# Kernel optimization log

Measured on AMD Instinct MI355X. Metric: run time of the kernel, lower is better.

## Reference

```python
import jax, jax.numpy as jnp
import numpy as np

N, E, M = 20000, 320000, 64
LOG2 = float(np.log(2.0))
INV_SQRT_M = 1.0 / float(np.sqrt(M))
PW_S = float(np.sqrt(1.0 / 5.0))   # path weight for 0e-output paths: sqrt(ir_out.dim / n_paths)
PW_V = float(np.sqrt(3.0 / 5.0))   # path weight for 1e-output paths
INV_SQRT3 = 1.0 / float(np.sqrt(3.0))
INV_SQRT2 = 1.0 / float(np.sqrt(2.0))


def ssp(x):  # ShiftedSoftPlus
    return jax.nn.softplus(x) - LOG2


def split(feat):
    return feat[:, :M], feat[:, M:].reshape(feat.shape[0], M, 3)


def e3_linear(feat, W0, b0, W1):
    # e3nn o3.Linear per irrep group, fan-in normalized; bias only on scalar (0e) irreps
    s, v = split(feat)
    s = s @ (W0 * INV_SQRT_M) + b0
    v = jnp.einsum('nui,uv->nvi', v, W1 * INV_SQRT_M)
    return jnp.concatenate([s, v.reshape(v.shape[0], 3 * M)], axis=-1)


def fcnet(h, Ws):
    # e3nn FullyConnectedNet: no biases, fan-in normalized, ssp between layers
    for i, W in enumerate(Ws):
        h = h @ (W * (1.0 / float(np.sqrt(W.shape[0]))))
        if i < len(Ws) - 1:
            h = ssp(h)
    return h


def setup_inputs() -> dict:
    key = jax.random.key(0)
    ks = jax.random.split(key, 24)
    r = lambda i, shape: jax.random.normal(ks[i], shape, dtype=jnp.float32)
    inp = {
        'x': r(0, (N, 4 * M)),
        'edge_index': jax.random.randint(ks[1], (2, E), 0, N, dtype=jnp.int64)
        if jax.config.jax_enable_x64 else jax.random.randint(ks[1], (2, E), 0, N),
        'edge_sh': r(2, (E, 4)),
        'edge_attr': r(3, (E, 64)),
        # linear_node_pre
        'W_pre0': r(4, (M, M)), 'b_pre0': jnp.zeros((M,), jnp.float32), 'W_pre1': r(5, (M, M)),
        # NormGate fc (plain torch nn.Linear with bias)
        'Wg1': r(6, (2 * M, 2 * M)) * 0.08, 'bg1': jnp.zeros((2 * M,), jnp.float32),
        'Wg2': r(7, (2 * M, 2 * M)) * 0.08, 'bg2': jnp.zeros((2 * M,), jnp.float32),
        # linear_node
        'Wn0': r(8, (M, M)), 'bn0': jnp.zeros((M,), jnp.float32), 'Wn1': r(9, (M, M)),
        # fc_node: [edge_attr_dim=64, 32, weight_numel=5*M]
        'Wf1': r(10, (64, 32)), 'Wf2': r(11, (32, 5 * M)),
        # layer_l0: [192, 32, 5*M]
        'Wl1': r(12, (192, 32)), 'Wl2': r(13, (32, 5 * M)),
        # linear_out
        'Wo0': r(14, (M, M)), 'bo0': jnp.zeros((M,), jnp.float32), 'Wo1': r(15, (M, M)),
    }
    return inp


def reference(x, edge_index, edge_sh, edge_attr,
              W_pre0, b_pre0, W_pre1, Wg1, bg1, Wg2, bg2,
              Wn0, bn0, Wn1, Wf1, Wf2, Wl1, Wl2, Wo0, bo0, Wo1):
    edge_dst, edge_src = edge_index[0], edge_index[1]

    # --- pre linear + edge invariants s0 ---
    pre_x = e3_linear(x, W_pre0, b_pre0, W_pre1)
    ps, pv = split(pre_x)
    # InnerProduct on 1e group (uuu, path weight 1/ir.dim): mean over m of elementwise product
    ip1 = jnp.einsum('eui,eui->eu', pv[edge_dst], pv[edge_src]) * (1.0 / 3.0)  # [E, M]
    s0 = jnp.concatenate([ps[edge_dst], ps[edge_dst], ip1], axis=-1)  # [E, 192]

    # --- NormGate ---
    xs, xv = split(x)
    norm_v = jnp.sqrt(jnp.sum(xv * xv, axis=-1) + 1e-12)  # [N, M]
    f0 = jnp.concatenate([xs, norm_v], axis=-1)  # [N, 2M]
    g = jax.nn.silu(f0 @ Wg1 + bg1) @ Wg2 + bg2  # [N, 2M]
    gated = xv * g[:, M:, None]
    xg = jnp.concatenate([g[:, :M], gated.reshape(N, 3 * M)], axis=-1)

    xg = e3_linear(xg, Wn0, bn0, Wn1)
    self_x = xg

    # --- per-edge tensor product weights ---
    w = (fcnet(edge_attr, [Wf1, Wf2]) * fcnet(s0, [Wl1, Wl2])).reshape(E, 5, M)

    # --- edge-wise equivariant tensor product (uvu, 5 paths) ---
    gs, gv = split(xg)
    es, ev = gs[edge_src], gv[edge_src]            # [E,M], [E,M,3]
    sh0, sh1 = edge_sh[:, 0], edge_sh[:, 1:4]      # [E], [E,3]

    out_s = PW_S * (w[:, 0] * es * sh0[:, None]
                    + w[:, 3] * jnp.einsum('eui,ei->eu', ev, sh1) * INV_SQRT3)
    cross = jnp.cross(ev, sh1[:, None, :])
    out_v = PW_V * (w[:, 1][:, :, None] * es[:, :, None] * sh1[:, None, :]
                    + w[:, 2][:, :, None] * ev * sh0[:, None, None]
                    + w[:, 4][:, :, None] * cross * INV_SQRT2)
    edge_feat = jnp.concatenate([out_s, out_v.reshape(E, 3 * M)], axis=-1)  # [E, 4M]

    # --- scatter aggregate to destination nodes ---
    out = jax.ops.segment_sum(edge_feat, edge_dst, num_segments=N)
    out = out + self_x  # irrep_in_node == irrep_out
    out = e3_linear(out, Wo0, bo0, Wo1)
    return out
```

## Files before the change

kernel.cpp:

```cpp
#include <hip/hip_runtime.h>
#include <math.h>

#define NNODE 20000
#define NEDGE 320000

__device__ __forceinline__ float sspf(float x) {
    return fmaxf(x, 0.f) + log1pf(expf(-fabsf(x))) - 0.6931471805599453f;
}

__global__ __launch_bounds__(256) void k_e3lin(
    const float* __restrict__ in, const float* __restrict__ add,
    float* __restrict__ out,
    const float* __restrict__ W0, const float* __restrict__ b0,
    const float* __restrict__ W1, int nrows)
{
    __shared__ float sW0[64 * 64];
    __shared__ float sW1[64 * 64];
    __shared__ float sb0[64];
    __shared__ float srow[4][256];
    const int tid = threadIdx.x;
    for (int i = tid; i < 64 * 16; i += 256) {
        ((float4*)sW0)[i] = ((const float4*)W0)[i];
        ((float4*)sW1)[i] = ((const float4*)W1)[i];
    }
    if (tid < 64) sb0[tid] = b0[tid];
    __syncthreads();

    const int rr = tid >> 6;
    const int v  = tid & 63;
    for (int r0 = blockIdx.x * 4; r0 < nrows; r0 += gridDim.x * 4) {
        {
            int i = tid;
            int r = i >> 6, c = i & 63;
            int row = r0 + r;
            float4 val = make_float4(0.f, 0.f, 0.f, 0.f);
            if (row < nrows) {
                val = ((const float4*)(in + (size_t)row * 256))[c];
                if (add) {
                    float4 a = ((const float4*)(add + (size_t)row * 256))[c];
                    val.x += a.x; val.y += a.y; val.z += a.z; val.w += a.w;
                }
            }
            ((float4*)srow[r])[c] = val;
        }
        __syncthreads();

        int row = r0 + rr;
        if (row < nrows) {
            const float* rw = srow[rr];
            float s = 0.f, a0 = 0.f, a1 = 0.f, a2 = 0.f;
            #pragma unroll 16
            for (int u = 0; u < 64; ++u) {
                float w0 = sW0[u * 64 + v];
                float w1 = sW1[u * 64 + v];
                s  += rw[u] * w0;
                a0 += rw[64 + u * 3 + 0] * w1;
                a1 += rw[64 + u * 3 + 1] * w1;
                a2 += rw[64 + u * 3 + 2] * w1;
            }
            out[row * 256 + v]              = s  * 0.125f + sb0[v];
            out[row * 256 + 64 + v * 3 + 0] = a0 * 0.125f;
            out[row * 256 + 64 + v * 3 + 1] = a1 * 0.125f;
            out[row * 256 + 64 + v * 3 + 2] = a2 * 0.125f;
        }
        __syncthreads();
    }
}

__global__ __launch_bounds__(256) void k_gate(
    const float* __restrict__ x, float* __restrict__ xg,
    const float* __restrict__ Wg1, const float* __restrict__ bg1,
    const float* __restrict__ Wg2, const float* __restrict__ bg2,
    int nrows)
{
    __shared__ float sW1[128 * 128];
    __shared__ float sW2[128 * 128];
    __shared__ float sb1[128], sb2[128];
    __shared__ float srow[2][256];
    __shared__ float sf0[2][128];
    __shared__ float sh1[2][128];
    const int tid = threadIdx.x;
    for (int i = tid; i < 128 * 32; i += 256) {
        ((float4*)sW1)[i] = ((const float4*)Wg1)[i];
        ((float4*)sW2)[i] = ((const float4*)Wg2)[i];
    }
    if (tid < 128) { sb1[tid] = bg1[tid]; sb2[tid] = bg2[tid]; }
    __syncthreads();

    const int rr = tid >> 7;
    const int j  = tid & 127;
    for (int base = blockIdx.x * 2; base < nrows; base += gridDim.x * 2) {
        if (tid < 128) {
            int r = tid >> 6, c = tid & 63;
            int row = base + r;
            float4 v = make_float4(0.f, 0.f, 0.f, 0.f);
            if (row < nrows) v = ((const float4*)(x + (size_t)row * 256))[c];
            ((float4*)srow[r])[c] = v;
        }
        __syncthreads();
        {
            float f;
            if (j < 64) f = srow[rr][j];
            else {
                int u = j - 64;
                float v0 = srow[rr][64 + u * 3 + 0];
                float v1 = srow[rr][64 + u * 3 + 1];
                float v2 = srow[rr][64 + u * 3 + 2];
                f = sqrtf(v0 * v0 + v1 * v1 + v2 * v2 + 1e-12f);
            }
            sf0[rr][j] = f;
        }
        __syncthreads();
        {
            float acc = sb1[j];
            #pragma unroll 16
            for (int k = 0; k < 128; ++k) acc += sf0[rr][k] * sW1[k * 128 + j];
            sh1[rr][j] = acc / (1.f + expf(-acc));
        }
        __syncthreads();
        {
            float acc = sb2[j];
            #pragma unroll 16
            for (int k = 0; k < 128; ++k) acc += sh1[rr][k] * sW2[k * 128 + j];
            int row = base + rr;
            if (row < nrows) {
                if (j < 64) xg[row * 256 + j] = acc;
                else {
                    int u = j - 64;
                    xg[row * 256 + 64 + u * 3 + 0] = srow[rr][64 + u * 3 + 0] * acc;
                    xg[row * 256 + 64 + u * 3 + 1] = srow[rr][64 + u * 3 + 1] * acc;
                    xg[row * 256 + 64 + u * 3 + 2] = srow[rr][64 + u * 3 + 2] * acc;
                }
            }
        }
        __syncthreads();
    }
}

__global__ __launch_bounds__(256) void k_hist(const int* __restrict__ ei, int* __restrict__ hist) {
    int e = blockIdx.x * 256 + threadIdx.x;
    if (e < NEDGE) atomicAdd(&hist[ei[e]], 1);
}

__global__ __launch_bounds__(1024) void k_scan(const int* __restrict__ hist,
                                               int* __restrict__ offs,
                                               int* __restrict__ curs) {
    __shared__ int part[1024];
    const int t = threadIdx.x;
    const int base = t * 20;
    int loc[20];
    int s = 0;
    #pragma unroll
    for (int k = 0; k < 20; ++k) {
        int b = base + k;
        int v = (b < NNODE) ? hist[b] : 0;
        loc[k] = s; s += v;
    }
    part[t] = s;
    __syncthreads();
    for (int off = 1; off < 1024; off <<= 1) {
        int v = (t >= off) ? part[t - off] : 0;
        __syncthreads();
        part[t] += v;
        __syncthreads();
    }
    int excl = (t == 0) ? 0 : part[t - 1];
    #pragma unroll
    for (int k = 0; k < 20; ++k) {
        int b = base + k;
        if (b < NNODE) { offs[b] = excl + loc[k]; curs[b] = excl + loc[k]; }
    }
    if (t == 1023) offs[NNODE] = part[1023];
}

__global__ __launch_bounds__(256) void k_scatteridx(const int* __restrict__ ei,
                                                    int* __restrict__ curs,
                                                    int* __restrict__ order) {
    int e = blockIdx.x * 256 + threadIdx.x;
    if (e < NEDGE) {
        int p = atomicAdd(&curs[ei[e]], 1);
        order[p] = e;
    }
}

#define EPW 2
__global__ __launch_bounds__(1024, 4) void k_edge(
    const float* __restrict__ pre, const float* __restrict__ slf,
    const int* __restrict__ ei, const float* __restrict__ eshp,
    const float* __restrict__ ea,
    const int* __restrict__ offs, const int* __restrict__ order,
    const float* __restrict__ Wf1, const float* __restrict__ Wf2,
    const float* __restrict__ Wl1, const float* __restrict__ Wl2,
    float* __restrict__ acc)
{
    __shared__ float2 sW1mb[64 * 64];
    __shared__ float4 sW2a[32 * 64];
    __shared__ float4 sW2b[32 * 64];
    __shared__ float2 sW2c[32 * 64];
    __shared__ float  sIN[16][EPW][192];
    __shared__ float  sH [16][EPW][64];
    const int tid = threadIdx.x;
    const float sc_f1 = 0.125f;
    const float sc_l1 = 0.07216878364870323f;
    const float sc_2  = 0.17677669529663687f;
    for (int i = tid; i < 64 * 64; i += 1024) {
        int u = i >> 6, c = i & 63, j = c & 31;
        float wm, wb;
        if (c < 32) {
            wm = Wf1[u * 32 + j] * sc_f1;
            wb = 0.f;
        } else {
            wm = (Wl1[u * 32 + j] + Wl1[(64 + u) * 32 + j]) * sc_l1;
            wb = Wl1[(128 + u) * 32 + j] * sc_l1;
        }
        sW1mb[i] = make_float2(wm, wb);
    }
    for (int i = tid; i < 32 * 64; i += 1024) {
        int jj = i >> 6, col = i & 63;
        const float* f2 = Wf2 + jj * 320 + col;
        const float* l2 = Wl2 + jj * 320 + col;
        sW2a[i] = make_float4(f2[0] * sc_2, f2[64] * sc_2, f2[128] * sc_2, f2[192] * sc_2);
        sW2b[i] = make_float4(l2[0] * sc_2, l2[64] * sc_2, l2[128] * sc_2, l2[192] * sc_2);
        sW2c[i] = make_float2(f2[256] * sc_2, l2[256] * sc_2);
    }
    __syncthreads();

    const int lane  = tid & 63;
    const int w     = tid >> 6;
    const int gwave = blockIdx.x * (blockDim.x >> 6) + w;
    const int nwav  = gridDim.x * (blockDim.x >> 6);
    const float* inb = &sIN[w][0][(lane >> 5) << 6];

    const float PW_S = 0.4472135954999579f;
    const float PW_V = 0.7745966692414834f;
    const float IS3  = 0.5773502691896258f;
    const float IS2  = 0.7071067811865476f;

    for (int d = gwave; d < NNODE; d += nwav) {
        const int e0 = __builtin_amdgcn_readfirstlane(offs[d]);
        const int e1 = __builtin_amdgcn_readfirstlane(offs[d + 1]);
        float psd = pre[d * 256 + lane];
        float pd0 = pre[d * 256 + 64 + lane * 3 + 0];
        float pd1 = pre[d * 256 + 64 + lane * 3 + 1];
        float pd2 = pre[d * 256 + 64 + lane * 3 + 2];
        sIN[w][0][64 + lane] = psd;
        sIN[w][1][64 + lane] = psd;

        float accS = 0.f, aV0 = 0.f, aV1 = 0.f, aV2 = 0.f;

        for (int i = e0; i < e1; i += EPW) {
            const int cnt = e1 - i;
            int eo[EPW], srcv[EPW];
            #pragma unroll
            for (int t = 0; t < EPW; ++t) {
                int idx = (t < cnt) ? (i + t) : i;
                int e = __builtin_amdgcn_readfirstlane(order[idx]);
                int s = __builtin_amdgcn_readfirstlane(ei[NEDGE + e]);
                eo[t] = e; srcv[t] = s;
                float ps0 = pre[s * 256 + 64 + lane * 3 + 0];
                float ps1 = pre[s * 256 + 64 + lane * 3 + 1];
                float ps2 = pre[s * 256 + 64 + lane * 3 + 2];
                float ip1 = (pd0 * ps0 + pd1 * ps1 + pd2 * ps2) * (1.f / 3.f);
                float eav = ea[e * 64 + lane];
                sIN[w][t][lane]       = eav;
                sIN[w][t][128 + lane] = ip1;
            }

            float hacc[EPW] = {0.f, 0.f};
            #pragma unroll 16
            for (int uu = 0; uu < 64; ++uu) {
                float2 wmb = sW1mb[uu * 64 + lane];
                #pragma unroll
                for (int t = 0; t < EPW; ++t) {
                    float b1 = inb[t * 192 + uu];
                    float bI = sIN[w][t][128 + uu];
                    hacc[t] += b1 * wmb.x + bI * wmb.y;
                }
            }
            #pragma unroll
            for (int t = 0; t < EPW; ++t) sH[w][t][lane] = sspf(hacc[t]);

            float aA[EPW][5], aB[EPW][5];
            #pragma unroll
            for (int t = 0; t < EPW; ++t)
                #pragma unroll
                for (int k = 0; k < 5; ++k) { aA[t][k] = 0.f; aB[t][k] = 0.f; }
            #pragma unroll 8
            for (int jj = 0; jj < 32; ++jj) {
                float4 wa = sW2a[jj * 64 + lane];
                float4 wb = sW2b[jj * 64 + lane];
                float2 wc = sW2c[jj * 64 + lane];
                #pragma unroll
                for (int t = 0; t < EPW; ++t) {
                    float hA = sH[w][t][jj];
                    float hB = sH[w][t][32 + jj];
                    aA[t][0] += hA * wa.x; aA[t][1] += hA * wa.y;
                    aA[t][2] += hA * wa.z; aA[t][3] += hA * wa.w;
                    aA[t][4] += hA * wc.x;
                    aB[t][0] += hB * wb.x; aB[t][1] += hB * wb.y;
                    aB[t][2] += hB * wb.z; aB[t][3] += hB * wb.w;
                    aB[t][4] += hB * wc.y;
                }
            }

            #pragma unroll
            for (int t = 0; t < EPW; ++t) {
                if (t >= cnt) break;
                int e = eo[t], s = srcv[t];
                float w0 = aA[t][0] * aB[t][0];
                float w1 = aA[t][1] * aB[t][1];
                float w2 = aA[t][2] * aB[t][2];
                float w3 = aA[t][3] * aB[t][3];
                float w4 = aA[t][4] * aB[t][4];
                float es  = slf[s * 256 + lane];
                float ev0 = slf[s * 256 + 64 + lane * 3 + 0];
                float ev1 = slf[s * 256 + 64 + lane * 3 + 1];
                float ev2 = slf[s * 256 + 64 + lane * 3 + 2];
                float s0v = eshp[e * 4 + 0];
                float sx  = eshp[e * 4 + 1];
                float sy  = eshp[e * 4 + 2];
                float sz  = eshp[e * 4 + 3];
                float dotv = ev0 * sx + ev1 * sy + ev2 * sz;
                accS += PW_S * (w0 * es * s0v + w3 * dotv * IS3);
                float cx = ev1 * sz - ev2 * sy;
                float cy = ev2 * sx - ev0 * sz;
                float cz = ev0 * sy - ev1 * sx;
                aV0 += PW_V * (w1 * es * sx + w2 * ev0 * s0v + w4 * cx * IS2);
                aV1 += PW_V * (w1 * es * sy + w2 * ev1 * s0v + w4 * cy * IS2);
                aV2 += PW_V * (w1 * es * sz + w2 * ev2 * s0v + w4 * cz * IS2);
            }
        }

        acc[d * 256 + lane]              = accS;
        acc[d * 256 + 64 + lane * 3 + 0] = aV0;
        acc[d * 256 + 64 + lane * 3 + 1] = aV1;
        acc[d * 256 + 64 + lane * 3 + 2] = aV2;
    }
}

extern "C" void kernel_launch(void* const* d_in, const int* in_sizes, int n_in,
                              void* d_out, int out_size, void* d_ws, size_t ws_size,
                              hipStream_t stream) {
    const float* x     = (const float*)d_in[0];
    const int*   ei    = (const int*)  d_in[1];
    const float* esh   = (const float*)d_in[2];
    const float* eattr = (const float*)d_in[3];
    const float* Wpre0 = (const float*)d_in[4];
    const float* bpre0 = (const float*)d_in[5];
    const float* Wpre1 = (const float*)d_in[6];
    const float* Wg1   = (const float*)d_in[7];
    const float* bg1   = (const float*)d_in[8];
    const float* Wg2   = (const float*)d_in[9];
    const float* bg2   = (const float*)d_in[10];
    const float* Wn0   = (const float*)d_in[11];
    const float* bn0   = (const float*)d_in[12];
    const float* Wn1   = (const float*)d_in[13];
    const float* Wf1   = (const float*)d_in[14];
    const float* Wf2   = (const float*)d_in[15];
    const float* Wl1   = (const float*)d_in[16];
    const float* Wl2   = (const float*)d_in[17];
    const float* Wo0   = (const float*)d_in[18];
    const float* bo0   = (const float*)d_in[19];
    const float* Wo1   = (const float*)d_in[20];
    float* out = (float*)d_out;
    float* ws  = (float*)d_ws;

    float* pre = ws;
    float* xg  = ws + (size_t)NNODE * 256;
    float* slf = ws + (size_t)NNODE * 256 * 2;
    float* acc = ws + (size_t)NNODE * 256 * 3;
    int*   hist  = (int*)(ws + (size_t)NNODE * 256 * 4);
    int*   offs  = hist + NNODE;
    int*   curs  = offs + NNODE + 2;
    int*   order = curs + NNODE;

    hipMemsetAsync(hist, 0, NNODE * sizeof(int), stream);
    k_hist      <<<(NEDGE + 255) / 256, 256, 0, stream>>>(ei, hist);
    k_scan      <<<1, 1024, 0, stream>>>(hist, offs, curs);
    k_scatteridx<<<(NEDGE + 255) / 256, 256, 0, stream>>>(ei, curs, order);

    k_e3lin<<<1280, 256, 0, stream>>>(x,  nullptr, pre, Wpre0, bpre0, Wpre1, NNODE);
    k_gate <<<512,  256, 0, stream>>>(x,  xg, Wg1, bg1, Wg2, bg2, NNODE);
    k_e3lin<<<1280, 256, 0, stream>>>(xg, nullptr, slf, Wn0, bn0, Wn1, NNODE);
    k_edge <<<256, 1024, 0, stream>>>(pre, slf, ei, esh, eattr, offs, order,
                                      Wf1, Wf2, Wl1, Wl2, acc);
    k_e3lin<<<1280, 256, 0, stream>>>(acc, slf, out, Wo0, bo0, Wo1, NNODE);
}
```

Measured before the change: 1.136 ms.

## Process four edges per wave and broadcast hidden values via readlane

Doubles the number of edges each wave handles per iteration, so every shared-memory weight load is reused across four edges instead of two. Replaces the shared-memory staging of the inner-product and hidden activations with cross-lane readlane broadcasts from registers, which removes LDS stores and loads and shrinks the per-wave shared buffers. The cost is more registers per thread, which may spill or cut occupancy under the 1024-thread launch bound, and more padding waste for nodes whose edge count is not a multiple of four.

```diff
diff --git a/kernel.cpp b/kernel.cpp
--- a/kernel.cpp
+++ b/kernel.cpp
@@ -6,6 +6,10 @@
 
 __device__ __forceinline__ float sspf(float x) {
     return fmaxf(x, 0.f) + log1pf(expf(-fabsf(x))) - 0.6931471805599453f;
+}
+
+__device__ __forceinline__ float rlf(float v, int l) {
+    return __int_as_float(__builtin_amdgcn_readlane(__float_as_int(v), l));
 }
 
 __global__ __launch_bounds__(256) void k_e3lin(
@@ -183,7 +187,7 @@
     }
 }
 
-#define EPW 2
+#define EPW 4
 __global__ __launch_bounds__(1024, 4) void k_edge(
     const float* __restrict__ pre, const float* __restrict__ slf,
     const int* __restrict__ ei, const float* __restrict__ eshp,
@@ -197,8 +201,8 @@
     __shared__ float4 sW2a[32 * 64];
     __shared__ float4 sW2b[32 * 64];
     __shared__ float2 sW2c[32 * 64];
-    __shared__ float  sIN[16][EPW][192];
-    __shared__ float  sH [16][EPW][64];
+    __shared__ float  sEAV[16][EPW][64];
+    __shared__ float  sPSD[16][64];
     const int tid = threadIdx.x;
     const float sc_f1 = 0.125f;
     const float sc_l1 = 0.07216878364870323f;
@@ -229,7 +233,12 @@
     const int w     = tid >> 6;
     const int gwave = blockIdx.x * (blockDim.x >> 6) + w;
     const int nwav  = gridDim.x * (blockDim.x >> 6);
-    const float* inb = &sIN[w][0][(lane >> 5) << 6];
+    const bool lo   = (lane < 32);
+
+    const float* inbp[EPW];
+    #pragma unroll
+    for (int t = 0; t < EPW; ++t)
+        inbp[t] = lo ? &sEAV[w][t][0] : &sPSD[w][0];
 
     const float PW_S = 0.4472135954999579f;
     const float PW_V = 0.7745966692414834f;
@@ -243,14 +252,14 @@
         float pd0 = pre[d * 256 + 64 + lane * 3 + 0];
         float pd1 = pre[d * 256 + 64 + lane * 3 + 1];
         float pd2 = pre[d * 256 + 64 + lane * 3 + 2];
-        sIN[w][0][64 + lane] = psd;
-        sIN[w][1][64 + lane] = psd;
+        sPSD[w][lane] = psd;
 
         float accS = 0.f, aV0 = 0.f, aV1 = 0.f, aV2 = 0.f;
 
         for (int i = e0; i < e1; i += EPW) {
             const int cnt = e1 - i;
             int eo[EPW], srcv[EPW];
+            float ip1[EPW];
             #pragma unroll
             for (int t = 0; t < EPW; ++t) {
                 int idx = (t < cnt) ? (i + t) : i;
@@ -260,25 +269,24 @@
                 float ps0 = pre[s * 256 + 64 + lane * 3 + 0];
                 float ps1 = pre[s * 256 + 64 + lane * 3 + 1];
                 float ps2 = pre[s * 256 + 64 + lane * 3 + 2];
-                float ip1 = (pd0 * ps0 + pd1 * ps1 + pd2 * ps2) * (1.f / 3.f);
-                float eav = ea[e * 64 + lane];
-                sIN[w][t][lane]       = eav;
-                sIN[w][t][128 + lane] = ip1;
-            }
-
-            float hacc[EPW] = {0.f, 0.f};
+                ip1[t] = (pd0 * ps0 + pd1 * ps1 + pd2 * ps2) * (1.f / 3.f);
+                sEAV[w][t][lane] = ea[e * 64 + lane];
+            }
+
+            float hacc[EPW] = {0.f, 0.f, 0.f, 0.f};
             #pragma unroll 16
             for (int uu = 0; uu < 64; ++uu) {
                 float2 wmb = sW1mb[uu * 64 + lane];
                 #pragma unroll
                 for (int t = 0; t < EPW; ++t) {
-                    float b1 = inb[t * 192 + uu];
-                    float bI = sIN[w][t][128 + uu];
+                    float b1 = inbp[t][uu];
+                    float bI = rlf(ip1[t], uu);
                     hacc[t] += b1 * wmb.x + bI * wmb.y;
                 }
             }
+            float hval[EPW];
             #pragma unroll
-            for (int t = 0; t < EPW; ++t) sH[w][t][lane] = sspf(hacc[t]);
+            for (int t = 0; t < EPW; ++t) hval[t] = sspf(hacc[t]);
 
             float aA[EPW][5], aB[EPW][5];
             #pragma unroll
@@ -292,8 +300,8 @@
                 float2 wc = sW2c[jj * 64 + lane];
                 #pragma unroll
                 for (int t = 0; t < EPW; ++t) {
-                    float hA = sH[w][t][jj];
-                    float hB = sH[w][t][32 + jj];
+                    float hA = rlf(hval[t], jj);
+                    float hB = rlf(hval[t], jj + 32);
                     aA[t][0] += hA * wa.x; aA[t][1] += hA * wa.y;
                     aA[t][2] += hA * wa.z; aA[t][3] += hA * wa.w;
                     aA[t][4] += hA * wc.x;
```

Result: slower. 1.178 ms (+3.7%).
